# Kernel optimization log

Measured on AMD Instinct MI355X. Metric: run time of the kernel, lower is better.

The kernel has to match this reference:

```python
import jax, jax.numpy as jnp
import numpy as np

INIT_VAL = 2.0
WS = 12
MASK_CONST = -50000.0
EPS = 1.1920929e-07  # torch.finfo(float32).eps


def poolsum(x, b, w, ws):
    """Windowed decay-weighted cumulative pooling, batch_first=False layout.
    x: (T, N, D), b: (T-1, N) in [0,1], w: (T, N) in (0,1].
    """
    T, N, D = x.shape
    dt = x.dtype
    xp = jnp.pad(x, ((ws - 1, 0), (0, 0), (0, 0)))            # (T+ws-1, N, D)
    x_win = jnp.stack([xp[i:i + T] for i in range(ws)], 0)     # (ws, T, N, D); x_win[i,t]=x[t+i-(ws-1)]
    bp = jnp.pad(b, ((ws - 1, 0), (0, 0)))                     # (T+ws-2, N)
    b_win = jnp.stack([bp[i:i + T] for i in range(ws - 1)], 0)  # (ws-1, T, N)
    b_win = jnp.concatenate([b_win, jnp.ones((1, T, N), dt)], 0)  # append ones row -> (ws, T, N)
    # coeffs[i] = prod_{j=i}^{ws-1} b_win[j]  (reverse cumprod)
    coeffs = jnp.flip(jnp.cumprod(jnp.flip(b_win, 0), axis=0), 0)
    wp = jnp.pad(w, ((ws - 1, 0), (0, 0)), constant_values=1.0)
    w_win = jnp.stack([wp[i:i + T] for i in range(ws)], 0)     # (ws, T, N)
    cw = coeffs * w_win
    x_acc = jnp.einsum('wtn,wtnd->tnd', cw, x_win)
    c = cw.sum(0)[..., None]
    return x_acc / c


def _forward(queries, keys, values):
    L, B, KV_H, D = keys.shape
    Q_H = queries.shape[2]
    G = Q_H // KV_H
    k = keys.reshape(L, B * KV_H, D)
    v = values.reshape(L, B * KV_H, D)
    # router on last channel of keys (eval path: straight-through decisions)
    router_logits = k[:, :, -1] - INIT_VAL
    probs = jax.nn.sigmoid(router_logits)
    dec = (probs > 0.5).astype(probs.dtype)
    router_probs = dec - jax.lax.stop_gradient(probs) + probs
    # per-token weights from mean of last channel of grouped query heads
    weight_logits = queries[..., -1].reshape(L, B, KV_H, G).mean(-1).reshape(L, B * KV_H)
    weights = jax.nn.sigmoid(weight_logits + INIT_VAL) + EPS
    pooled = poolsum(jnp.concatenate([k, v], axis=-1), router_probs[1:], weights, WS)
    k2 = pooled[:, :, :D].reshape(L, B, KV_H, D)
    v2 = pooled[:, :, D:].reshape(L, B, KV_H, D)
    rp = router_probs.reshape(L, B, KV_H)
    # eval attn score mask, shifted left by one with zero row appended
    mask = rp * MASK_CONST
    mask = jnp.concatenate([mask[1:], jnp.zeros((1, B, KV_H), mask.dtype)], axis=0)
    # eval path zeroes last channel of q and pooled k
    q_out = queries.at[..., -1].set(0.0)
    k2 = k2.at[..., -1].set(0.0)
    # GQA expansion (optimized_attn_bias=True path)
    k2 = jnp.repeat(k2, G, axis=2)
    v2 = jnp.repeat(v2, G, axis=2)
    mask = jnp.repeat(mask, G, axis=2)
    return q_out, k2, v2, mask


def setup_inputs() -> dict:
    key = jax.random.key(0)
    kq, kk, kv = jax.random.split(key, 3)
    L, B, Q_H, KV_H, D = 2048, 4, 32, 8, 128
    return {
        'queries': jax.random.normal(kq, (L, B, Q_H, D), jnp.float32),
        'keys': jax.random.normal(kk, (L, B, KV_H, D), jnp.float32),
        'values': jax.random.normal(kv, (L, B, KV_H, D), jnp.float32),
    }


def reference(queries, keys, values):
    return _forward(queries, keys, values)
```

## Files before the change

kernel.cpp:

```cpp
#include <hip/hip_runtime.h>
#include <math.h>

#define L 2048
#define B 4
#define QH 32
#define KVH 8
#define G 4
#define D 128
#define NS (B*KVH)
#define WS 12
#define MASK_CONST -50000.0f
#define EPS_F 1.1920929e-07f

#define NQ_BLOCKS   32768
#define NPOOL_BLOCKS 16384
#define NMASK_BLOCKS 1024

typedef float f32x4 __attribute__((ext_vector_type(4)));

__global__ void fused_kernel(const f32x4* __restrict__ q4,
                             const float* __restrict__ q,
                             const float* __restrict__ k, const float* __restrict__ v,
                             f32x4* __restrict__ outq4,
                             float* __restrict__ k2, float* __restrict__ v2,
                             float* __restrict__ mask) {
    int bid = blockIdx.x;
    if (bid < NQ_BLOCKS) {
        size_t i = (size_t)bid * 256 + threadIdx.x;
        f32x4 val = __builtin_nontemporal_load(&q4[i]);
        if ((i & (D / 4 - 1)) == (D / 4 - 1)) val.w = 0.0f;
        __builtin_nontemporal_store(val, &outq4[i]);
    } else if (bid < NQ_BLOCKS + NPOOL_BLOCKS) {
        int pb = bid - NQ_BLOCKS;
        int n  = pb & (NS - 1);
        int t0 = (pb >> 5) * 4;
        int b = n >> 3, h = n & 7;
        int tid  = threadIdx.x;
        int grp  = tid >> 6;
        int lane = tid & 63;

        __shared__ float s_w[15];
        __shared__ float s_dec[14];

        if (tid < 60) {
            int i = tid >> 2, g = tid & 3;
            int s = t0 - 11 + i;
            float pv = 0.0f;
            if (s >= 0)
                pv = q[(((size_t)s * B + b) * QH + h * G + g) * D + (D - 1)];
            pv += __shfl_xor(pv, 1);
            pv += __shfl_xor(pv, 2);
            if (g == 0)
                s_w[i] = 1.0f / (1.0f + __expf(-(pv * 0.25f + 2.0f))) + EPS_F;
        } else if (tid >= 64 && tid < 78) {
            int u = t0 - 10 + (tid - 64);
            float kv = (u >= 0) ? k[((size_t)u * NS + n) * D + (D - 1)] : 3.0f;
            s_dec[tid - 64] = (kv > 2.0f) ? 1.0f : 0.0f;
        }
        __syncthreads();

        int t = t0 + grp;
        int c = lane * 4;
        const bool is_k = (c < D);
        const float* base = is_k ? k : v;
        int coff = is_k ? c : (c - D);

        float ax = 0.f, ay = 0.f, az = 0.f, aw = 0.f, den = 0.f;
        for (int j = 0; j < WS; ++j) {
            int s = t - j;
            if (s < 0) break;
            int wi = grp + 11 - j;
            if (j > 0 && s_dec[wi] == 0.0f) break;
            float w = s_w[wi];
            const f32x4 x = *reinterpret_cast<const f32x4*>(base + ((size_t)s * NS + n) * D + coff);
            ax += w * x.x; ay += w * x.y; az += w * x.z; aw += w * x.w;
            den += w;
        }
        f32x4 o;
        o.x = ax / den; o.y = ay / den; o.z = az / den; o.w = aw / den;

        size_t head0 = (((size_t)t * B + b) * QH + h * G) * D;
        if (is_k) {
            if (c == D - 4) o.w = 0.0f;
            f32x4* dst = reinterpret_cast<f32x4*>(k2) + (head0 + c) / 4;
            __builtin_nontemporal_store(o, dst);
            __builtin_nontemporal_store(o, dst + D / 4);
            __builtin_nontemporal_store(o, dst + 2 * (D / 4));
            __builtin_nontemporal_store(o, dst + 3 * (D / 4));
        } else {
            f32x4* dst = reinterpret_cast<f32x4*>(v2) + (head0 + (c - D)) / 4;
            __builtin_nontemporal_store(o, dst);
            __builtin_nontemporal_store(o, dst + D / 4);
            __builtin_nontemporal_store(o, dst + 2 * (D / 4));
            __builtin_nontemporal_store(o, dst + 3 * (D / 4));
        }
    } else {
        int idx = (bid - NQ_BLOCKS - NPOOL_BLOCKS) * 256 + threadIdx.x;
        int qh = idx & (QH - 1);
        int b = (idx >> 5) & (B - 1);
        int t = idx >> 7;
        float m = 0.0f;
        if (t < L - 1) {
            int n = b * KVH + (qh >> 2);
            float kv = k[((size_t)(t + 1) * NS + n) * D + (D - 1)];
            m = (kv > 2.0f) ? MASK_CONST : 0.0f;
        }
        mask[idx] = m;
    }
}

extern "C" void kernel_launch(void* const* d_in, const int* in_sizes, int n_in,
                              void* d_out, int out_size, void* d_ws, size_t ws_size,
                              hipStream_t stream) {
    const float* q = (const float*)d_in[0];
    const float* k = (const float*)d_in[1];
    const float* v = (const float*)d_in[2];

    float* out_q    = (float*)d_out;
    float* out_k2   = out_q  + (size_t)L * B * QH * D;
    float* out_v2   = out_k2 + (size_t)L * B * QH * D;
    float* out_mask = out_v2 + (size_t)L * B * QH * D;

    int blocks = NQ_BLOCKS + NPOOL_BLOCKS + NMASK_BLOCKS;
    fused_kernel<<<blocks, 256, 0, stream>>>(
        (const f32x4*)q, q, k, v,
        (f32x4*)out_q, out_k2, out_v2, out_mask);
}
```

Before: 104.6 us.

## Pool 16 timesteps per block, fold mask into pool blocks, reorder block ranges

Each pooling block now covers 16 timesteps, with each 64-thread group looping over 4 of them. This cuts the number of pool blocks and amortises the shared weight and decision loads over more outputs. The separate mask blocks are removed: the mask is written from the already-computed s_dec values inside the pool blocks. Pool blocks are also scheduled before the q-copy blocks. The cost is less parallelism per pooling block and a serial per-thread loop over timesteps.

```diff
diff --git a/kernel.cpp b/kernel.cpp
--- a/kernel.cpp
+++ b/kernel.cpp
@@ -12,9 +12,9 @@
 #define MASK_CONST -50000.0f
 #define EPS_F 1.1920929e-07f
 
+#define TBLK 16
+#define NPOOL_BLOCKS ((L/TBLK)*NS)
 #define NQ_BLOCKS   32768
-#define NPOOL_BLOCKS 16384
-#define NMASK_BLOCKS 1024
 
 typedef float f32x4 __attribute__((ext_vector_type(4)));
 
@@ -25,24 +25,18 @@
                              float* __restrict__ k2, float* __restrict__ v2,
                              float* __restrict__ mask) {
     int bid = blockIdx.x;
-    if (bid < NQ_BLOCKS) {
-        size_t i = (size_t)bid * 256 + threadIdx.x;
-        f32x4 val = __builtin_nontemporal_load(&q4[i]);
-        if ((i & (D / 4 - 1)) == (D / 4 - 1)) val.w = 0.0f;
-        __builtin_nontemporal_store(val, &outq4[i]);
-    } else if (bid < NQ_BLOCKS + NPOOL_BLOCKS) {
-        int pb = bid - NQ_BLOCKS;
-        int n  = pb & (NS - 1);
-        int t0 = (pb >> 5) * 4;
+    if (bid < NPOOL_BLOCKS) {
+        int n  = bid & (NS - 1);
+        int t0 = (bid >> 5) * TBLK;
         int b = n >> 3, h = n & 7;
         int tid  = threadIdx.x;
         int grp  = tid >> 6;
         int lane = tid & 63;
 
-        __shared__ float s_w[15];
-        __shared__ float s_dec[14];
+        __shared__ float s_w[27];
+        __shared__ float s_dec[27];
 
-        if (tid < 60) {
+        if (tid < 108) {
             int i = tid >> 2, g = tid & 3;
             int s = t0 - 11 + i;
             float pv = 0.0f;
@@ -52,60 +46,64 @@
             pv += __shfl_xor(pv, 2);
             if (g == 0)
                 s_w[i] = 1.0f / (1.0f + __expf(-(pv * 0.25f + 2.0f))) + EPS_F;
-        } else if (tid >= 64 && tid < 78) {
-            int u = t0 - 10 + (tid - 64);
-            float kv = (u >= 0) ? k[((size_t)u * NS + n) * D + (D - 1)] : 3.0f;
-            s_dec[tid - 64] = (kv > 2.0f) ? 1.0f : 0.0f;
+        } else if (tid >= 128 && tid < 155) {
+            int u = t0 - 10 + (tid - 128);
+            float kv = (u >= 0 && u < L) ? k[((size_t)u * NS + n) * D + (D - 1)] : 3.0f;
+            s_dec[tid - 128] = (kv > 2.0f) ? 1.0f : 0.0f;
         }
         __syncthreads();
 
-        int t = t0 + grp;
         int c = lane * 4;
         const bool is_k = (c < D);
         const float* base = is_k ? k : v;
         int coff = is_k ? c : (c - D);
 
-        float ax = 0.f, ay = 0.f, az = 0.f, aw = 0.f, den = 0.f;
-        for (int j = 0; j < WS; ++j) {
-            int s = t - j;
-            if (s < 0) break;
-            int wi = grp + 11 - j;
-            if (j > 0 && s_dec[wi] == 0.0f) break;
-            float w = s_w[wi];
-            const f32x4 x = *reinterpret_cast<const f32x4*>(base + ((size_t)s * NS + n) * D + coff);
-            ax += w * x.x; ay += w * x.y; az += w * x.z; aw += w * x.w;
-            den += w;
+        for (int it = 0; it < 4; ++it) {
+            int lt = grp * 4 + it;
+            int t  = t0 + lt;
+
+            float ax = 0.f, ay = 0.f, az = 0.f, aw = 0.f, den = 0.f;
+            for (int j = 0; j < WS; ++j) {
+                int s = t - j;
+                if (s < 0) break;
+                int wi = lt - j + 11;
+                if (j > 0 && s_dec[wi] == 0.0f) break;
+                float w = s_w[wi];
+                const f32x4 x = *reinterpret_cast<const f32x4*>(base + ((size_t)s * NS + n) * D + coff);
+                ax += w * x.x; ay += w * x.y; az += w * x.z; aw += w * x.w;
+                den += w;
+            }
+            f32x4 o;
+            o.x = ax / den; o.y = ay / den; o.z = az / den; o.w = aw / den;
+
+            size_t head0 = (((size_t)t * B + b) * QH + h * G) * D;
+            if (is_k) {
+                if (c == D - 4) o.w = 0.0f;
+                f32x4* dst = reinterpret_cast<f32x4*>(k2) + (head0 + c) / 4;
+                __builtin_nontemporal_store(o, dst);
+                __builtin_nontemporal_store(o, dst + D / 4);
+                __builtin_nontemporal_store(o, dst + 2 * (D / 4));
+                __builtin_nontemporal_store(o, dst + 3 * (D / 4));
+            } else {
+                f32x4* dst = reinterpret_cast<f32x4*>(v2) + (head0 + (c - D)) / 4;
+                __builtin_nontemporal_store(o, dst);
+                __builtin_nontemporal_store(o, dst + D / 4);
+                __builtin_nontemporal_store(o, dst + 2 * (D / 4));
+                __builtin_nontemporal_store(o, dst + 3 * (D / 4));
+            }
         }
-        f32x4 o;
-        o.x = ax / den; o.y = ay / den; o.z = az / den; o.w = aw / den;
 
-        size_t head0 = (((size_t)t * B + b) * QH + h * G) * D;
-        if (is_k) {
-            if (c == D - 4) o.w = 0.0f;
-            f32x4* dst = reinterpret_cast<f32x4*>(k2) + (head0 + c) / 4;
-            __builtin_nontemporal_store(o, dst);
-            __builtin_nontemporal_store(o, dst + D / 4);
-            __builtin_nontemporal_store(o, dst + 2 * (D / 4));
-            __builtin_nontemporal_store(o, dst + 3 * (D / 4));
-        } else {
-            f32x4* dst = reinterpret_cast<f32x4*>(v2) + (head0 + (c - D)) / 4;
-            __builtin_nontemporal_store(o, dst);
-            __builtin_nontemporal_store(o, dst + D / 4);
-            __builtin_nontemporal_store(o, dst + 2 * (D / 4));
-            __builtin_nontemporal_store(o, dst + 3 * (D / 4));
+        if (tid < TBLK * G) {
+            int lt = tid >> 2, g = tid & 3;
+            int t = t0 + lt;
+            float m = (t < L - 1) ? s_dec[lt + 11] * MASK_CONST : 0.0f;
+            mask[(size_t)t * B * QH + b * QH + h * G + g] = m;
         }
     } else {
-        int idx = (bid - NQ_BLOCKS - NPOOL_BLOCKS) * 256 + threadIdx.x;
-        int qh = idx & (QH - 1);
-        int b = (idx >> 5) & (B - 1);
-        int t = idx >> 7;
-        float m = 0.0f;
-        if (t < L - 1) {
-            int n = b * KVH + (qh >> 2);
-            float kv = k[((size_t)(t + 1) * NS + n) * D + (D - 1)];
-            m = (kv > 2.0f) ? MASK_CONST : 0.0f;
-        }
-        mask[idx] = m;
+        size_t i = (size_t)(bid - NPOOL_BLOCKS) * 256 + threadIdx.x;
+        f32x4 val = __builtin_nontemporal_load(&q4[i]);
+        if ((i & (D / 4 - 1)) == (D / 4 - 1)) val.w = 0.0f;
+        __builtin_nontemporal_store(val, &outq4[i]);
     }
 }
 
@@ -121,7 +119,7 @@
     float* out_v2   = out_k2 + (size_t)L * B * QH * D;
     float* out_mask = out_v2 + (size_t)L * B * QH * D;
 
-    int blocks = NQ_BLOCKS + NPOOL_BLOCKS + NMASK_BLOCKS;
+    int blocks = NPOOL_BLOCKS + NQ_BLOCKS;
     fused_kernel<<<blocks, 256, 0, stream>>>(
         (const f32x4*)q, q, k, v,
         (f32x4*)out_q, out_k2, out_v2, out_mask);
```

After: 99.17 us. -5.2%, faster.
